# Optimization experiments

Measured on AMD Instinct MI355X. Metric: run time of the kernel, lower is better.

## Reference

```python
import jax, jax.numpy as jnp
import numpy as np

D = 196  # input_size
B = 262144

def _lrelu(x):
    return jax.nn.leaky_relu(x, 0.1)

def setup_inputs() -> dict:
    key = jax.random.key(0)
    ks = jax.random.split(key, 24)
    def w(k, shape):
        fan_in = shape[0]
        return jax.random.uniform(k, shape, jnp.float32, -1.0, 1.0) / np.sqrt(fan_in)
    inp = {}
    inp['x'] = jax.random.normal(ks[0], (B, D), jnp.float32)
    # feature attention: D -> D//2 -> D
    inp['fa_w1'] = w(ks[1], (D, D // 2)); inp['fa_b1'] = jnp.zeros((D // 2,), jnp.float32)
    inp['fa_w2'] = w(ks[2], (D // 2, D)); inp['fa_b2'] = jnp.zeros((D,), jnp.float32)
    # encoder: D -> 96 -> 64 -> 32 -> (8 mean, 8 logvar)
    inp['e_w1'] = w(ks[3], (D, 96)); inp['e_b1'] = jnp.zeros((96,), jnp.float32)
    inp['e_w2'] = w(ks[4], (96, 64)); inp['e_b2'] = jnp.zeros((64,), jnp.float32)
    inp['e_w3'] = w(ks[5], (64, 32)); inp['e_b3'] = jnp.zeros((32,), jnp.float32)
    inp['e_wm'] = w(ks[6], (32, 8)); inp['e_bm'] = jnp.zeros((8,), jnp.float32)
    inp['e_wv'] = w(ks[7], (32, 8)); inp['e_bv'] = jnp.zeros((8,), jnp.float32)
    # decoder: 8 -> 32 -> 64 -> 96 -> D
    inp['d_w1'] = w(ks[8], (8, 32)); inp['d_b1'] = jnp.zeros((32,), jnp.float32)
    inp['d_w2'] = w(ks[9], (32, 64)); inp['d_b2'] = jnp.zeros((64,), jnp.float32)
    inp['d_w3'] = w(ks[10], (64, 96)); inp['d_b3'] = jnp.zeros((96,), jnp.float32)
    inp['d_w4'] = w(ks[11], (96, D)); inp['d_b4'] = jnp.zeros((D,), jnp.float32)
    # layer attention: 3 -> 3 + softmax
    inp['la_w'] = w(ks[12], (3, 3)); inp['la_b'] = jnp.zeros((3,), jnp.float32)
    return inp

def _decoder(z, d_w1, d_b1, d_w2, d_b2, d_w3, d_b3, d_w4, d_b4):
    z = _lrelu(z @ d_w1 + d_b1)
    z = _lrelu(z @ d_w2 + d_b2)
    z = _lrelu(z @ d_w3 + d_b3)
    return jax.nn.sigmoid(z @ d_w4 + d_b4)

def reference(x, fa_w1, fa_b1, fa_w2, fa_b2,
              e_w1, e_b1, e_w2, e_b2, e_w3, e_b3, e_wm, e_bm, e_wv, e_bv,
              d_w1, d_b1, d_w2, d_b2, d_w3, d_b3, d_w4, d_b4,
              la_w, la_b):
    # feature attention
    a = jax.nn.sigmoid(jnp.tanh(x @ fa_w1 + fa_b1) @ fa_w2 + fa_b2)
    attn_weights = a / (jnp.mean(a, axis=1, keepdims=True) + 1e-8)
    x_attn = x * attn_weights
    # encoder
    h1 = _lrelu(x_attn @ e_w1 + e_b1)   # [B,96]
    h2 = _lrelu(h1 @ e_w2 + e_b2)       # [B,64]
    h3 = _lrelu(h2 @ e_w3 + e_b3)       # [B,32]
    mean = h3 @ e_wm + e_bm             # [B,8]
    log_var = h3 @ e_wv + e_bv          # [B,8]
    std = jnp.exp(0.5 * log_var)
    # reparameterize (fresh eps per call, matching torch.randn_like per call)
    ek = jax.random.split(jax.random.key(42), 4)
    z = mean + jax.random.normal(ek[0], mean.shape, mean.dtype) * std
    recon = _decoder(z, d_w1, d_b1, d_w2, d_b2, d_w3, d_b3, d_w4, d_b4)
    # per-layer losses: decoder re-invoked with fresh reparam each time
    layer_losses = []
    for i, h in enumerate((h1, h2, h3)):
        zi = mean + jax.random.normal(ek[i + 1], mean.shape, mean.dtype) * std
        lr = _decoder(zi, d_w1, d_b1, d_w2, d_b2, d_w3, d_b3, d_w4, d_b4)
        layer_losses.append(jnp.mean((h - lr[:, :h.shape[1]]) ** 2, axis=1))
    layer_losses = jnp.stack(layer_losses, axis=1)  # [B,3]
    layer_attn = jax.nn.softmax(layer_losses @ la_w + la_b, axis=-1)
    weighted_layer_loss = jnp.mean(jnp.sum(layer_losses * layer_attn, axis=1))
    return (recon, mean, log_var, attn_weights, weighted_layer_loss)
```

## Files before the change

kernel.cpp:

```cpp
#include <hip/hip_runtime.h>
#include <cstdint>
#include <cstddef>


typedef short short8 __attribute__((ext_vector_type(8)));
typedef float f32x4  __attribute__((ext_vector_type(4)));
typedef float f32x16 __attribute__((ext_vector_type(16)));
typedef unsigned short u16x4 __attribute__((ext_vector_type(4)));
typedef uint32_t u32x2 __attribute__((ext_vector_type(2)));

static constexpr size_t OFF_RECON = 0;
static constexpr size_t OFF_MEAN  = (size_t)262144 * 196;
static constexpr size_t OFF_LOGV  = OFF_MEAN + (size_t)262144 * 8;
static constexpr size_t OFF_ATTN  = OFF_LOGV + (size_t)262144 * 8;
static constexpr size_t OFF_LOSS  = OFF_ATTN + (size_t)262144 * 196;

static constexpr int WS_FA1 = 0;
static constexpr int WS_FA2 = 26624;
static constexpr int WS_E1  = 51712;
static constexpr int WS_E2  = 71680;
static constexpr int WS_E3  = 78848;
static constexpr int WS_EMV = 81408;
static constexpr int WS_D1  = 82944;
static constexpr int WS_D2  = 83456;
static constexpr int WS_D3  = 86528;
static constexpr int WS_D4  = 94208;
static constexpr int WS_TOT = 119296;

static constexpr int XA0 = 0;
static constexpr int T0  = 6656;
static constexpr int TA0 = 10240;
static constexpr int Zo  = 0;
static constexpr int D1o = 2048;
static constexpr int D2o = 5120;
static constexpr int D3o = 10240;
static constexpr int H1o = 17408;
static constexpr int H2o = 20992;
static constexpr int H3o = 23552;
static constexpr int SU_TOT = 25088;

static constexpr int SF_MEAN = 0;
static constexpr int SF_STD  = 256;
static constexpr int SF_ATT  = 512;
static constexpr int SF_LL   = 544;
static constexpr int SF_TOT  = 640;

static constexpr unsigned short BF_ONE = 0x3F80;

struct Params {
  const float* x;
  const float* fa_w1; const float* fa_b1; const float* fa_w2; const float* fa_b2;
  const float* e_w1;  const float* e_b1;  const float* e_w2;  const float* e_b2;
  const float* e_w3;  const float* e_b3;  const float* e_wm;  const float* e_bm;
  const float* e_wv;  const float* e_bv;
  const float* d_w1;  const float* d_b1;  const float* d_w2;  const float* d_b2;
  const float* d_w3;  const float* d_b3;  const float* d_w4;  const float* d_b4;
  const float* la_w;  const float* la_b;
  float* out;
  uint32_t key[8];
};

__host__ __device__ inline void tf2x32(uint32_t k0, uint32_t k1, uint32_t x0, uint32_t x1,
                                       uint32_t& o0, uint32_t& o1)
{
  uint32_t kx = k0 ^ k1 ^ 0x1BD11BDAu;
  uint32_t a = x0 + k0, b = x1 + k1;
#define TF_R(r) { a += b; b = (b << (r)) | (b >> (32 - (r))); b ^= a; }
  TF_R(13) TF_R(15) TF_R(26) TF_R(6)
  a += k1; b += kx + 1u;
  TF_R(17) TF_R(29) TF_R(16) TF_R(24)
  a += kx; b += k0 + 2u;
  TF_R(13) TF_R(15) TF_R(26) TF_R(6)
  a += k0; b += k1 + 3u;
  TF_R(17) TF_R(29) TF_R(16) TF_R(24)
  a += k1; b += kx + 4u;
  TF_R(13) TF_R(15) TF_R(26) TF_R(6)
  a += kx; b += k0 + 5u;
#undef TF_R
  o0 = a; o1 = b;
}

__device__ __forceinline__ float jax_normal(uint32_t k0, uint32_t k1, uint32_t idx)
{
  uint32_t o0, o1;
  tf2x32(k0, k1, 0u, idx, o0, o1);
  uint32_t bits = o0 ^ o1;
  float f = __uint_as_float((bits >> 9) | 0x3f800000u) - 1.0f;
  const float lo = -0.99999994f;
  float u = fmaf(f, 2.0f, lo);
  u = fmaxf(u, lo);
  float w = -log1pf(-u * u);
  float p;
  if (w < 5.0f) {
    w -= 2.5f;
    p = 2.81022636e-08f;
    p = fmaf(p, w, 3.43273939e-07f);
    p = fmaf(p, w, -3.5233877e-06f);
    p = fmaf(p, w, -4.39150654e-06f);
    p = fmaf(p, w, 0.00021858087f);
    p = fmaf(p, w, -0.00125372503f);
    p = fmaf(p, w, -0.00417768164f);
    p = fmaf(p, w, 0.246640727f);
    p = fmaf(p, w, 1.50140941f);
  } else {
    w = sqrtf(w) - 3.0f;
    p = -0.000200214257f;
    p = fmaf(p, w, 0.000100950558f);
    p = fmaf(p, w, 0.00134934322f);
    p = fmaf(p, w, -0.00367342844f);
    p = fmaf(p, w, 0.00573950773f);
    p = fmaf(p, w, -0.0076224613f);
    p = fmaf(p, w, 0.00943887047f);
    p = fmaf(p, w, 1.00167406f);
    p = fmaf(p, w, 2.83297682f);
  }
  return 1.41421356237f * (p * u);
}

__host__ __device__ __forceinline__ unsigned short f2b(float f) {
  uint32_t u = __float_as_uint(f);
  uint32_t r = u + 0x7fffu + ((u >> 16) & 1u);
  return (unsigned short)(r >> 16);
}
__device__ __forceinline__ float b2f(unsigned short hh) {
  return __uint_as_float(((uint32_t)hh) << 16);
}
__device__ __forceinline__ uint32_t cvt_pk(float lo, float hi) {
  uint32_t r;
  asm("v_cvt_pk_bf16_f32 %0, %1, %2" : "=v"(r) : "v"(lo), "v"(hi));
  return r;
}
__device__ __forceinline__ float rcpf(float x) { return __builtin_amdgcn_rcpf(x); }
__device__ __forceinline__ float sigm(float x) { return rcpf(1.0f + __expf(-x)); }
__device__ __forceinline__ float tanh_fast(float x) {
  float xc = fminf(fmaxf(x, -8.0f), 8.0f);
  float t = __expf(2.0f * xc);
  return (t - 1.0f) * rcpf(t + 1.0f);
}

__global__ void pack_w(Params p, unsigned short* ws)
{
  int e = blockIdx.x * 256 + threadIdx.x;
  if (e >= WS_TOT) return;
  int base, KS, K, N, special = 0;
  const float* src = nullptr; const float* bias = nullptr;
  if (e < WS_FA2)      { base = WS_FA1; KS = 13; K = 196; N = 98;  src = p.fa_w1; bias = p.fa_b1; }
  else if (e < WS_E1)  { base = WS_FA2; KS = 7;  K = 98;  N = 196; src = p.fa_w2; bias = p.fa_b2; }
  else if (e < WS_E2)  { base = WS_E1;  KS = 13; K = 196; N = 96;  src = p.e_w1;  bias = p.e_b1; }
  else if (e < WS_E3)  { base = WS_E2;  KS = 7;  K = 96;  N = 64;  src = p.e_w2;  bias = p.e_b2; }
  else if (e < WS_EMV) { base = WS_E3;  KS = 5;  K = 64;  N = 32;  src = p.e_w3;  bias = p.e_b3; }
  else if (e < WS_D1)  { base = WS_EMV; KS = 3;  K = 32;  N = 16;  special = 1; }
  else if (e < WS_D2)  { base = WS_D1;  KS = 1;  K = 8;   N = 32;  src = p.d_w1;  bias = p.d_b1; }
  else if (e < WS_D3)  { base = WS_D2;  KS = 3;  K = 32;  N = 64;  src = p.d_w2;  bias = p.d_b2; }
  else if (e < WS_D4)  { base = WS_D3;  KS = 5;  K = 64;  N = 96;  src = p.d_w3;  bias = p.d_b3; }
  else                 { base = WS_D4;  KS = 7;  K = 96;  N = 196; src = p.d_w4;  bias = p.d_b4; }
  int local = e - base;
  int j = local & 7, lane = (local >> 3) & 63, t = local >> 9;
  int ksi = t % KS, ft = t / KS;
  int k = ksi * 16 + ((lane >> 5) << 3) + j;
  int n = ft * 32 + (lane & 31);
  float v = 0.f;
  if (n < N) {
    if (k < K)       v = special ? ((n < 8) ? p.e_wm[k * 8 + n] : p.e_wv[k * 8 + (n - 8)])
                                 : src[k * N + n];
    else if (k == K) v = special ? ((n < 8) ? p.e_bm[n] : p.e_bv[n - 8]) : bias[n];
  }
  ws[e] = f2b(v);
}

template<int KS>
__device__ __forceinline__ f32x16 tile32(const unsigned short* A, int sA,
                                         const unsigned short* W, int ft, int lane)
{
  f32x16 acc = {};
  const unsigned short* ar = A + (lane & 31) * sA + ((lane >> 5) << 3);
  const unsigned short* wp = W + (size_t)(ft * KS * 64 + lane) * 8;
#pragma unroll
  for (int ks = 0; ks < KS; ++ks) {
    short8 bv  = *(const short8*)(ar + ks * 16);
    short8 wv8 = *(const short8*)(wp + ks * 512);
    acc = __builtin_amdgcn_mfma_f32_32x32x16_bf16(wv8, bv, acc, 0, 0, 0);
  }
  return acc;
}

template<int KS, int MT, int NFT>
__device__ __forceinline__ void layer32(unsigned short* sUb, int aOff, int sA,
                                        int dOff, int sD,
                                        const unsigned short* W, int lane, int wv)
{
  const int m = lane & 31, h = lane >> 5;
  for (int t = wv; t < MT * NFT; t += 4) {
    int mt = (MT == 1) ? 0 : (t & (MT - 1));
    int ft = (MT == 1) ? t : (t >> (MT == 2 ? 1 : 0));
    f32x16 acc = tile32<KS>(sUb + aOff + mt * 32 * sA, sA, W, ft, lane);
    int rr = mt * 32 + m;
#pragma unroll
    for (int g = 0; g < 4; ++g) {
      float v0 = fmaxf(acc[4*g+0], 0.1f * acc[4*g+0]);
      float v1 = fmaxf(acc[4*g+1], 0.1f * acc[4*g+1]);
      float v2 = fmaxf(acc[4*g+2], 0.1f * acc[4*g+2]);
      float v3 = fmaxf(acc[4*g+3], 0.1f * acc[4*g+3]);
      u32x2 pk = { cvt_pk(v0, v1), cvt_pk(v2, v3) };
      *(u32x2*)&sUb[dOff + rr * sD + ft * 32 + 8 * g + 4 * h] = pk;
    }
  }
}

__launch_bounds__(256, 3)
__global__ void vae_fused(Params p, const unsigned short* ws)
{
  __shared__ unsigned short sU[SU_TOT];
  __shared__ float sF[SF_TOT];
  unsigned short* sUb = sU;

  const int tid = threadIdx.x;
  const int lane = tid & 63;
  const int wv = tid >> 6;
  const int m = lane & 31;
  const int h = lane >> 5;
  const int rb0 = blockIdx.x * 32;

  if (tid < 128) sF[SF_ATT + tid] = 0.f;
  for (int idx = tid; idx < 1568; idx += 256) {
    int row = idx / 49, q = idx - row * 49;
    f32x4 xv = *(const f32x4*)(p.x + (size_t)(rb0 + row) * 196 + 4 * q);
    u32x2 pk = { cvt_pk(xv[0], xv[1]), cvt_pk(xv[2], xv[3]) };
    *(u32x2*)&sUb[XA0 + row * 208 + 4 * q] = pk;
  }
  if (tid < 32) {
    unsigned short* r = sUb + XA0 + tid * 208;
    r[196] = BF_ONE; r[197] = 0; r[198] = 0; r[199] = 0;
    u16x4 z4 = {0, 0, 0, 0};
    *(u16x4*)&r[200] = z4; *(u16x4*)&r[204] = z4;
  }
  __syncthreads();

  {
    int ft = wv;
    f32x16 acc = tile32<13>(sUb + XA0, 208, ws + WS_FA1, ft, lane);
    if (ft < 3) {
#pragma unroll
      for (int g = 0; g < 4; ++g) {
        float v0 = tanh_fast(acc[4*g+0]), v1 = tanh_fast(acc[4*g+1]);
        float v2 = tanh_fast(acc[4*g+2]), v3 = tanh_fast(acc[4*g+3]);
        u32x2 pk = { cvt_pk(v0, v1), cvt_pk(v2, v3) };
        *(u32x2*)&sUb[T0 + m * 112 + ft * 32 + 8 * g + 4 * h] = pk;
      }
    } else if (h == 0) {
      *(uint32_t*)&sUb[T0 + m * 112 + 96] = cvt_pk(tanh_fast(acc[0]), tanh_fast(acc[1]));
    }
    if (tid < 32) {
      unsigned short* r = sUb + T0 + tid * 112;
      r[98] = BF_ONE; r[99] = 0;
      u16x4 z4 = {0, 0, 0, 0};
      *(u16x4*)&r[100] = z4; *(u16x4*)&r[104] = z4; *(u16x4*)&r[108] = z4;
    }
  }
  __syncthreads();

  for (int ft = wv; ft < 7; ft += 4) {
    f32x16 acc = tile32<7>(sUb + T0, 112, ws + WS_FA2, ft, lane);
    float s = 0.f;
#pragma unroll
    for (int g = 0; g < 4; ++g) {
      int fb = ft * 32 + 8 * g + 4 * h;
      if (fb <= 192) {
        float a0 = sigm(acc[4*g+0]), a1 = sigm(acc[4*g+1]);
        float a2 = sigm(acc[4*g+2]), a3 = sigm(acc[4*g+3]);
        s += a0 + a1 + a2 + a3;
        u32x2 pk = { cvt_pk(a0, a1), cvt_pk(a2, a3) };
        *(u32x2*)&sUb[TA0 + m * 200 + fb] = pk;
      }
    }
    s += __shfl_xor(s, 32, 64);
    if (lane < 32) atomicAdd(&sF[SF_ATT + m], s);
  }
  __syncthreads();

  for (int idx = tid; idx < 1568; idx += 256) {
    int row = idx / 49, q = idx - row * 49;
    float inv = rcpf(sF[SF_ATT + row] * (1.0f / 196.0f) + 1e-8f);
    u16x4 ah = *(const u16x4*)&sUb[TA0 + row * 200 + 4 * q];
    u16x4 xh = *(const u16x4*)&sUb[XA0 + row * 208 + 4 * q];
    f32x4 aw;
    float xo[4];
#pragma unroll
    for (int i = 0; i < 4; ++i) {
      aw[i] = b2f(ah[i]) * inv;
      xo[i] = b2f(xh[i]) * aw[i];
    }
    __builtin_nontemporal_store(aw, (f32x4*)(p.out + OFF_ATTN + (size_t)(rb0 + row) * 196 + 4 * q));
    u32x2 pk = { cvt_pk(xo[0], xo[1]), cvt_pk(xo[2], xo[3]) };
    *(u32x2*)&sUb[XA0 + row * 208 + 4 * q] = pk;
  }
  __syncthreads();

  layer32<13, 1, 3>(sUb, XA0, 208, H1o, 112, ws + WS_E1, lane, wv);
  if (tid < 32) {
    unsigned short* r = sUb + H1o + tid * 112;
    r[96] = BF_ONE; r[97] = 0; r[98] = 0; r[99] = 0;
    u16x4 z4 = {0, 0, 0, 0};
    *(u16x4*)&r[100] = z4; *(u16x4*)&r[104] = z4; *(u16x4*)&r[108] = z4;
  }
  __syncthreads();
  layer32<7, 1, 2>(sUb, H1o, 112, H2o, 80, ws + WS_E2, lane, wv);
  if (tid < 32) {
    unsigned short* r = sUb + H2o + tid * 80;
    r[64] = BF_ONE; r[65] = 0; r[66] = 0; r[67] = 0;
    u16x4 z4 = {0, 0, 0, 0};
    *(u16x4*)&r[68] = z4; *(u16x4*)&r[72] = z4; *(u16x4*)&r[76] = z4;
  }
  __syncthreads();
  layer32<5, 1, 1>(sUb, H2o, 80, H3o, 48, ws + WS_E3, lane, wv);
  if (tid < 32) {
    unsigned short* r = sUb + H3o + tid * 48;
    r[32] = BF_ONE; r[33] = 0; r[34] = 0; r[35] = 0;
    u16x4 z4 = {0, 0, 0, 0};
    *(u16x4*)&r[36] = z4; *(u16x4*)&r[40] = z4; *(u16x4*)&r[44] = z4;
  }
  __syncthreads();

  if (wv == 0) {
    f32x16 acc = tile32<3>(sUb + H3o, 48, ws + WS_EMV, 0, lane);
    f32x4 mv, lv;
#pragma unroll
    for (int e = 0; e < 4; ++e) { mv[e] = acc[e]; lv[e] = acc[4 + e]; }
#pragma unroll
    for (int e = 0; e < 4; ++e) {
      sF[SF_MEAN + m * 8 + 4 * h + e] = mv[e];
      sF[SF_STD  + m * 8 + 4 * h + e] = __expf(0.5f * lv[e]);
    }
    __builtin_nontemporal_store(mv, (f32x4*)(p.out + OFF_MEAN + (size_t)(rb0 + m) * 8 + 4 * h));
    __builtin_nontemporal_store(lv, (f32x4*)(p.out + OFF_LOGV + (size_t)(rb0 + m) * 8 + 4 * h));
  }
  __syncthreads();

  {
    int r = tid >> 1, half = tid & 1;
    int draw = r >> 5, row = r & 31;
    float z[4];
#pragma unroll
    for (int e = 0; e < 4; ++e) {
      int jj = 4 * half + e;
      float eps = jax_normal(p.key[2 * draw], p.key[2 * draw + 1],
                             (uint32_t)(rb0 + row) * 8u + (uint32_t)jj);
      z[e] = fmaf(eps, sF[SF_STD + row * 8 + jj], sF[SF_MEAN + row * 8 + jj]);
    }
    u32x2 pk = { cvt_pk(z[0], z[1]), cvt_pk(z[2], z[3]) };
    *(u32x2*)&sUb[Zo + r * 16 + 4 * half] = pk;
    if (tid < 128) {
      u16x4 one4 = {BF_ONE, 0, 0, 0}, z4 = {0, 0, 0, 0};
      *(u16x4*)&sUb[Zo + tid * 16 + 8]  = one4;
      *(u16x4*)&sUb[Zo + tid * 16 + 12] = z4;
    }
  }
  __syncthreads();

#pragma unroll
  for (int pass = 0; pass < 2; ++pass) {
    const int zr = pass * 64;
    layer32<1, 2, 1>(sUb, Zo + zr * 16, 16, D1o, 48, ws + WS_D1, lane, wv);
    if (pass == 0 && tid < 64) {
      unsigned short* r = sUb + D1o + tid * 48;
      r[32] = BF_ONE; r[33] = 0; r[34] = 0; r[35] = 0;
      u16x4 z4 = {0, 0, 0, 0};
      *(u16x4*)&r[36] = z4; *(u16x4*)&r[40] = z4; *(u16x4*)&r[44] = z4;
    }
    __syncthreads();
    layer32<3, 2, 2>(sUb, D1o, 48, D2o, 80, ws + WS_D2, lane, wv);
    if (pass == 0 && tid < 64) {
      unsigned short* r = sUb + D2o + tid * 80;
      r[64] = BF_ONE; r[65] = 0; r[66] = 0; r[67] = 0;
      u16x4 z4 = {0, 0, 0, 0};
      *(u16x4*)&r[68] = z4; *(u16x4*)&r[72] = z4; *(u16x4*)&r[76] = z4;
    }
    __syncthreads();
    layer32<5, 2, 3>(sUb, D2o, 80, D3o, 112, ws + WS_D3, lane, wv);
    if (pass == 0 && tid < 64) {
      unsigned short* r = sUb + D3o + tid * 112;
      r[96] = BF_ONE; r[97] = 0; r[98] = 0; r[99] = 0;
      u16x4 z4 = {0, 0, 0, 0};
      *(u16x4*)&r[100] = z4; *(u16x4*)&r[104] = z4; *(u16x4*)&r[108] = z4;
    }
    __syncthreads();

    auto d4_loss = [&](int dp, int ft, int hOff, int sH, float invD, int li) {
      f32x16 acc = tile32<7>(sUb + D3o + dp * 32 * 112, 112, ws + WS_D4, ft, lane);
      float s = 0.f;
#pragma unroll
      for (int g = 0; g < 4; ++g) {
        int fb = ft * 32 + 8 * g + 4 * h;
        u16x4 hh = *(const u16x4*)&sUb[hOff + m * sH + fb];
#pragma unroll
        for (int e = 0; e < 4; ++e) {
          float lr = sigm(acc[4 * g + e]);
          float d = b2f(hh[e]) - lr;
          s = fmaf(d, d, s);
        }
      }
      s += __shfl_xor(s, 32, 64);
      if (lane < 32) atomicAdd(&sF[SF_LL + li * 32 + m], s * invD);
    };

    if (pass == 0) {
      for (int t = wv; t < 10; t += 4) {
        if (t < 7) {
          f32x16 acc = tile32<7>(sUb + D3o, 112, ws + WS_D4, t, lane);
#pragma unroll
          for (int g = 0; g < 4; ++g) {
            int fb = t * 32 + 8 * g + 4 * h;
            if (fb <= 192) {
              f32x4 v;
#pragma unroll
              for (int e = 0; e < 4; ++e) v[e] = sigm(acc[4 * g + e]);
              __builtin_nontemporal_store(v,
                  (f32x4*)(p.out + OFF_RECON + (size_t)(rb0 + m) * 196 + fb));
            }
          }
        } else {
          d4_loss(1, t - 7, H1o, 112, 1.0f / 96.0f, 0);
        }
      }
    } else {
      for (int t = wv; t < 3; t += 4) {
        if (t < 2) d4_loss(0, t, H2o, 80, 1.0f / 64.0f, 1);
        else       d4_loss(1, 0, H3o, 48, 1.0f / 32.0f, 2);
      }
    }
    __syncthreads();
  }

  if (tid < 32) {
    int r = tid;
    float l0 = sF[SF_LL + r], l1 = sF[SF_LL + 32 + r], l2 = sF[SF_LL + 64 + r];
    float lg[3];
#pragma unroll
    for (int i = 0; i < 3; ++i)
      lg[i] = p.la_b[i] + l0 * p.la_w[0 * 3 + i] + l1 * p.la_w[1 * 3 + i] + l2 * p.la_w[2 * 3 + i];
    float mx = fmaxf(lg[0], fmaxf(lg[1], lg[2]));
    float e0 = __expf(lg[0] - mx), e1 = __expf(lg[1] - mx), e2 = __expf(lg[2] - mx);
    float inv = rcpf(e0 + e1 + e2);
    float wll = (l0 * e0 + l1 * e1 + l2 * e2) * inv;
#pragma unroll
    for (int mm = 1; mm <= 16; mm <<= 1) wll += __shfl_xor(wll, mm, 64);
    if (tid == 0) atomicAdd(p.out + OFF_LOSS, wll * (1.0f / 262144.0f));
  }
}

extern "C" void kernel_launch(void* const* d_in, const int* in_sizes, int n_in,
                              void* d_out, int out_size, void* d_ws, size_t ws_size,
                              hipStream_t stream)
{
  (void)in_sizes; (void)n_in; (void)ws_size; (void)out_size;
  Params p;
  p.x     = (const float*)d_in[0];
  p.fa_w1 = (const float*)d_in[1];  p.fa_b1 = (const float*)d_in[2];
  p.fa_w2 = (const float*)d_in[3];  p.fa_b2 = (const float*)d_in[4];
  p.e_w1  = (const float*)d_in[5];  p.e_b1  = (const float*)d_in[6];
  p.e_w2  = (const float*)d_in[7];  p.e_b2  = (const float*)d_in[8];
  p.e_w3  = (const float*)d_in[9];  p.e_b3  = (const float*)d_in[10];
  p.e_wm  = (const float*)d_in[11]; p.e_bm  = (const float*)d_in[12];
  p.e_wv  = (const float*)d_in[13]; p.e_bv  = (const float*)d_in[14];
  p.d_w1  = (const float*)d_in[15]; p.d_b1  = (const float*)d_in[16];
  p.d_w2  = (const float*)d_in[17]; p.d_b2  = (const float*)d_in[18];
  p.d_w3  = (const float*)d_in[19]; p.d_b3  = (const float*)d_in[20];
  p.d_w4  = (const float*)d_in[21]; p.d_b4  = (const float*)d_in[22];
  p.la_w  = (const float*)d_in[23]; p.la_b  = (const float*)d_in[24];
  p.out   = (float*)d_out;

  for (uint32_t j = 0; j < 4; ++j) {
    uint32_t o0, o1;
    tf2x32(0u, 42u, 0u, j, o0, o1);
    p.key[2 * j] = o0; p.key[2 * j + 1] = o1;
  }

  hipMemsetAsync((char*)d_out + OFF_LOSS * sizeof(float), 0, sizeof(float), stream);

  unsigned short* ws = (unsigned short*)d_ws;
  pack_w<<<(WS_TOT + 255) / 256, 256, 0, stream>>>(p, ws);
  vae_fused<<<262144 / 32, 256, 0, stream>>>(p, ws);
}
```

Baseline: 352.1 us.

## Shrink LDS footprint, pipeline decoder draws one at a time, raise occupancy

Reorganizes shared memory by aliasing encoder and decoder buffers and processing the four decoder draws one 32-row tile at a time instead of two 64-row passes. This cuts LDS use so the launch bound can rise from 3 to 4 blocks per CU. The next draw's first decoder layer is overlapped with the current draw's output layer, and eps generation is hoisted ahead of a barrier. Long-K MFMA chains now alternate between two accumulators to break the dependency. In exchange there are more barriers per block and a risk of register pressure or spills under the tighter bound.

New measurement: 355.3 us. About the same (+0.9%).

```diff
diff --git a/kernel.cpp b/kernel.cpp
--- a/kernel.cpp
+++ b/kernel.cpp
@@ -28,22 +28,18 @@
 static constexpr int WS_TOT = 119296;
 
 static constexpr int XA0 = 0;
-static constexpr int T0  = 6656;
-static constexpr int TA0 = 10240;
-static constexpr int Zo  = 0;
-static constexpr int D1o = 2048;
-static constexpr int D2o = 5120;
-static constexpr int D3o = 10240;
-static constexpr int H1o = 17408;
-static constexpr int H2o = 20992;
-static constexpr int H3o = 23552;
-static constexpr int SU_TOT = 25088;
-
-static constexpr int SF_MEAN = 0;
-static constexpr int SF_STD  = 256;
-static constexpr int SF_ATT  = 512;
-static constexpr int SF_LL   = 544;
-static constexpr int SF_TOT  = 640;
+static constexpr int T0  = 6912;
+static constexpr int TA0 = 10752;
+static constexpr int H1o = 6912;
+static constexpr int H2o = 10752;
+static constexpr int H3o = 13568;
+static constexpr int D1o = 15360;
+static constexpr int D2o = 3840;
+static constexpr int D3o = 0;
+static constexpr int Zo  = 17152;
+static constexpr int SU_TOT = 19200;
+static constexpr int SF_MEAN = 0, SF_STD = 256, SF_ATT = 512, SF_LL = 544;
+static constexpr int SF_TOT = 640;
 
 static constexpr unsigned short BF_ONE = 0x3F80;
 
@@ -172,47 +168,45 @@
 __device__ __forceinline__ f32x16 tile32(const unsigned short* A, int sA,
                                          const unsigned short* W, int ft, int lane)
 {
-  f32x16 acc = {};
+  f32x16 a0 = {}, a1 = {};
   const unsigned short* ar = A + (lane & 31) * sA + ((lane >> 5) << 3);
   const unsigned short* wp = W + (size_t)(ft * KS * 64 + lane) * 8;
 #pragma unroll
   for (int ks = 0; ks < KS; ++ks) {
     short8 bv  = *(const short8*)(ar + ks * 16);
     short8 wv8 = *(const short8*)(wp + ks * 512);
-    acc = __builtin_amdgcn_mfma_f32_32x32x16_bf16(wv8, bv, acc, 0, 0, 0);
-  }
-  return acc;
-}
-
-template<int KS, int MT, int NFT>
-__device__ __forceinline__ void layer32(unsigned short* sUb, int aOff, int sA,
-                                        int dOff, int sD,
-                                        const unsigned short* W, int lane, int wv)
+    if (KS >= 7 && (ks & 1)) a1 = __builtin_amdgcn_mfma_f32_32x32x16_bf16(wv8, bv, a1, 0, 0, 0);
+    else                     a0 = __builtin_amdgcn_mfma_f32_32x32x16_bf16(wv8, bv, a0, 0, 0, 0);
+  }
+  if (KS >= 7) a0 += a1;
+  return a0;
+}
+
+template<int KS, int NFT, int SA, int SD>
+__device__ __forceinline__ void layer_lrelu(unsigned short* sU, int aOff, int dOff,
+                                            const unsigned short* W, int lane, int wv)
 {
   const int m = lane & 31, h = lane >> 5;
-  for (int t = wv; t < MT * NFT; t += 4) {
-    int mt = (MT == 1) ? 0 : (t & (MT - 1));
-    int ft = (MT == 1) ? t : (t >> (MT == 2 ? 1 : 0));
-    f32x16 acc = tile32<KS>(sUb + aOff + mt * 32 * sA, sA, W, ft, lane);
-    int rr = mt * 32 + m;
-#pragma unroll
-    for (int g = 0; g < 4; ++g) {
-      float v0 = fmaxf(acc[4*g+0], 0.1f * acc[4*g+0]);
-      float v1 = fmaxf(acc[4*g+1], 0.1f * acc[4*g+1]);
-      float v2 = fmaxf(acc[4*g+2], 0.1f * acc[4*g+2]);
-      float v3 = fmaxf(acc[4*g+3], 0.1f * acc[4*g+3]);
+  for (int t = wv; t < NFT; t += 4) {
+    f32x16 acc = tile32<KS>(sU + aOff, SA, W, t, lane);
+#pragma unroll
+    for (int g = 0; g < 4; ++g) {
+      int fb = t * 32 + 8 * g + 4 * h;
+      float v0 = fmaxf(acc[4*g+0], 0.1f*acc[4*g+0]);
+      float v1 = fmaxf(acc[4*g+1], 0.1f*acc[4*g+1]);
+      float v2 = fmaxf(acc[4*g+2], 0.1f*acc[4*g+2]);
+      float v3 = fmaxf(acc[4*g+3], 0.1f*acc[4*g+3]);
       u32x2 pk = { cvt_pk(v0, v1), cvt_pk(v2, v3) };
-      *(u32x2*)&sUb[dOff + rr * sD + ft * 32 + 8 * g + 4 * h] = pk;
-    }
-  }
-}
-
-__launch_bounds__(256, 3)
+      *(u32x2*)&sU[dOff + m * SD + fb] = pk;
+    }
+  }
+}
+
+__launch_bounds__(256, 4)
 __global__ void vae_fused(Params p, const unsigned short* ws)
 {
   __shared__ unsigned short sU[SU_TOT];
   __shared__ float sF[SF_TOT];
-  unsigned short* sUb = sU;
 
   const int tid = threadIdx.x;
   const int lane = tid & 63;
@@ -221,56 +215,57 @@
   const int h = lane >> 5;
   const int rb0 = blockIdx.x * 32;
 
+  const u16x4 one4 = {BF_ONE, 0, 0, 0};
+  const u16x4 zr4  = {0, 0, 0, 0};
+
   if (tid < 128) sF[SF_ATT + tid] = 0.f;
   for (int idx = tid; idx < 1568; idx += 256) {
     int row = idx / 49, q = idx - row * 49;
     f32x4 xv = *(const f32x4*)(p.x + (size_t)(rb0 + row) * 196 + 4 * q);
     u32x2 pk = { cvt_pk(xv[0], xv[1]), cvt_pk(xv[2], xv[3]) };
-    *(u32x2*)&sUb[XA0 + row * 208 + 4 * q] = pk;
-  }
-  if (tid < 32) {
-    unsigned short* r = sUb + XA0 + tid * 208;
-    r[196] = BF_ONE; r[197] = 0; r[198] = 0; r[199] = 0;
-    u16x4 z4 = {0, 0, 0, 0};
-    *(u16x4*)&r[200] = z4; *(u16x4*)&r[204] = z4;
+    *(u32x2*)&sU[XA0 + row * 216 + 4 * q] = pk;
+  }
+  if (tid < 32) {
+    unsigned short* r = sU + XA0 + tid * 216;
+    *(u16x4*)&r[196] = one4; *(u16x4*)&r[200] = zr4; *(u16x4*)&r[204] = zr4;
+  }
+  if (tid < 128) {
+    unsigned short* r = sU + Zo + tid * 16;
+    *(u16x4*)&r[8] = one4; *(u16x4*)&r[12] = zr4;
   }
   __syncthreads();
 
   {
-    int ft = wv;
-    f32x16 acc = tile32<13>(sUb + XA0, 208, ws + WS_FA1, ft, lane);
-    if (ft < 3) {
-#pragma unroll
-      for (int g = 0; g < 4; ++g) {
-        float v0 = tanh_fast(acc[4*g+0]), v1 = tanh_fast(acc[4*g+1]);
-        float v2 = tanh_fast(acc[4*g+2]), v3 = tanh_fast(acc[4*g+3]);
+    int t = wv;
+    f32x16 acc = tile32<13>(sU + XA0, 216, ws + WS_FA1, t, lane);
+#pragma unroll
+    for (int g = 0; g < 4; ++g) {
+      int fb = t * 32 + 8 * g + 4 * h;
+      if (fb + 4 <= 120) {
+        float v0 = tanh_fast(acc[4*g+0]);
+        float v1 = tanh_fast(acc[4*g+1]);
+        float v2 = tanh_fast(acc[4*g+2]);
+        float v3 = tanh_fast(acc[4*g+3]);
+        if (fb == 96) v2 = 1.0f;
         u32x2 pk = { cvt_pk(v0, v1), cvt_pk(v2, v3) };
-        *(u32x2*)&sUb[T0 + m * 112 + ft * 32 + 8 * g + 4 * h] = pk;
+        *(u32x2*)&sU[T0 + m * 120 + fb] = pk;
       }
-    } else if (h == 0) {
-      *(uint32_t*)&sUb[T0 + m * 112 + 96] = cvt_pk(tanh_fast(acc[0]), tanh_fast(acc[1]));
-    }
-    if (tid < 32) {
-      unsigned short* r = sUb + T0 + tid * 112;
-      r[98] = BF_ONE; r[99] = 0;
-      u16x4 z4 = {0, 0, 0, 0};
-      *(u16x4*)&r[100] = z4; *(u16x4*)&r[104] = z4; *(u16x4*)&r[108] = z4;
-    }
-  }
-  __syncthreads();
-
-  for (int ft = wv; ft < 7; ft += 4) {
-    f32x16 acc = tile32<7>(sUb + T0, 112, ws + WS_FA2, ft, lane);
+    }
+  }
+  __syncthreads();
+
+  for (int t = wv; t < 7; t += 4) {
+    f32x16 acc = tile32<7>(sU + T0, 120, ws + WS_FA2, t, lane);
     float s = 0.f;
 #pragma unroll
     for (int g = 0; g < 4; ++g) {
-      int fb = ft * 32 + 8 * g + 4 * h;
-      if (fb <= 192) {
+      int fb = t * 32 + 8 * g + 4 * h;
+      if (fb + 4 <= 200) {
         float a0 = sigm(acc[4*g+0]), a1 = sigm(acc[4*g+1]);
         float a2 = sigm(acc[4*g+2]), a3 = sigm(acc[4*g+3]);
-        s += a0 + a1 + a2 + a3;
+        if (fb < 196) s += a0 + a1 + a2 + a3;
         u32x2 pk = { cvt_pk(a0, a1), cvt_pk(a2, a3) };
-        *(u32x2*)&sUb[TA0 + m * 200 + fb] = pk;
+        *(u32x2*)&sU[TA0 + m * 200 + fb] = pk;
       }
     }
     s += __shfl_xor(s, 32, 64);
@@ -281,8 +276,8 @@
   for (int idx = tid; idx < 1568; idx += 256) {
     int row = idx / 49, q = idx - row * 49;
     float inv = rcpf(sF[SF_ATT + row] * (1.0f / 196.0f) + 1e-8f);
-    u16x4 ah = *(const u16x4*)&sUb[TA0 + row * 200 + 4 * q];
-    u16x4 xh = *(const u16x4*)&sUb[XA0 + row * 208 + 4 * q];
+    u16x4 ah = *(const u16x4*)&sU[TA0 + row * 200 + 4 * q];
+    u16x4 xh = *(const u16x4*)&sU[XA0 + row * 216 + 4 * q];
     f32x4 aw;
     float xo[4];
 #pragma unroll
@@ -292,37 +287,34 @@
     }
     __builtin_nontemporal_store(aw, (f32x4*)(p.out + OFF_ATTN + (size_t)(rb0 + row) * 196 + 4 * q));
     u32x2 pk = { cvt_pk(xo[0], xo[1]), cvt_pk(xo[2], xo[3]) };
-    *(u32x2*)&sUb[XA0 + row * 208 + 4 * q] = pk;
-  }
-  __syncthreads();
-
-  layer32<13, 1, 3>(sUb, XA0, 208, H1o, 112, ws + WS_E1, lane, wv);
-  if (tid < 32) {
-    unsigned short* r = sUb + H1o + tid * 112;
-    r[96] = BF_ONE; r[97] = 0; r[98] = 0; r[99] = 0;
-    u16x4 z4 = {0, 0, 0, 0};
-    *(u16x4*)&r[100] = z4; *(u16x4*)&r[104] = z4; *(u16x4*)&r[108] = z4;
-  }
-  __syncthreads();
-  layer32<7, 1, 2>(sUb, H1o, 112, H2o, 80, ws + WS_E2, lane, wv);
-  if (tid < 32) {
-    unsigned short* r = sUb + H2o + tid * 80;
-    r[64] = BF_ONE; r[65] = 0; r[66] = 0; r[67] = 0;
-    u16x4 z4 = {0, 0, 0, 0};
-    *(u16x4*)&r[68] = z4; *(u16x4*)&r[72] = z4; *(u16x4*)&r[76] = z4;
-  }
-  __syncthreads();
-  layer32<5, 1, 1>(sUb, H2o, 80, H3o, 48, ws + WS_E3, lane, wv);
-  if (tid < 32) {
-    unsigned short* r = sUb + H3o + tid * 48;
-    r[32] = BF_ONE; r[33] = 0; r[34] = 0; r[35] = 0;
-    u16x4 z4 = {0, 0, 0, 0};
-    *(u16x4*)&r[36] = z4; *(u16x4*)&r[40] = z4; *(u16x4*)&r[44] = z4;
+    *(u32x2*)&sU[XA0 + row * 216 + 4 * q] = pk;
+  }
+  __syncthreads();
+
+  layer_lrelu<13, 3, 216, 120>(sU, XA0, H1o, ws + WS_E1, lane, wv);
+  if (tid < 32) {
+    unsigned short* r = sU + H1o + tid * 120;
+    *(u16x4*)&r[96] = one4; *(u16x4*)&r[100] = zr4;
+    *(u16x4*)&r[104] = zr4; *(u16x4*)&r[108] = zr4;
+  }
+  __syncthreads();
+  layer_lrelu<7, 2, 120, 88>(sU, H1o, H2o, ws + WS_E2, lane, wv);
+  if (tid < 32) {
+    unsigned short* r = sU + H2o + tid * 88;
+    *(u16x4*)&r[64] = one4; *(u16x4*)&r[68] = zr4;
+    *(u16x4*)&r[72] = zr4;  *(u16x4*)&r[76] = zr4;
+  }
+  __syncthreads();
+  layer_lrelu<5, 1, 88, 56>(sU, H2o, H3o, ws + WS_E3, lane, wv);
+  if (tid < 32) {
+    unsigned short* r = sU + H3o + tid * 56;
+    *(u16x4*)&r[32] = one4; *(u16x4*)&r[36] = zr4;
+    *(u16x4*)&r[40] = zr4;  *(u16x4*)&r[44] = zr4;
   }
   __syncthreads();
 
   if (wv == 0) {
-    f32x16 acc = tile32<3>(sUb + H3o, 48, ws + WS_EMV, 0, lane);
+    f32x16 acc = tile32<3>(sU + H3o, 56, ws + WS_EMV, 0, lane);
     f32x4 mv, lv;
 #pragma unroll
     for (int e = 0; e < 4; ++e) { mv[e] = acc[e]; lv[e] = acc[4 + e]; }
@@ -334,99 +326,104 @@
     __builtin_nontemporal_store(mv, (f32x4*)(p.out + OFF_MEAN + (size_t)(rb0 + m) * 8 + 4 * h));
     __builtin_nontemporal_store(lv, (f32x4*)(p.out + OFF_LOGV + (size_t)(rb0 + m) * 8 + 4 * h));
   }
-  __syncthreads();
-
+  if (tid < 32) {
+    unsigned short* r1 = sU + D1o + tid * 56;
+    *(u16x4*)&r1[32] = one4; *(u16x4*)&r1[36] = zr4;
+    *(u16x4*)&r1[40] = zr4;  *(u16x4*)&r1[44] = zr4;
+    unsigned short* r2 = sU + D2o + tid * 88;
+    *(u16x4*)&r2[64] = one4; *(u16x4*)&r2[68] = zr4;
+    *(u16x4*)&r2[72] = zr4;  *(u16x4*)&r2[76] = zr4;
+    unsigned short* r3 = sU + D3o + tid * 120;
+    *(u16x4*)&r3[96] = one4; *(u16x4*)&r3[100] = zr4;
+    *(u16x4*)&r3[104] = zr4; *(u16x4*)&r3[108] = zr4;
+  }
+  float eps4[4];
   {
-    int r = tid >> 1, half = tid & 1;
-    int draw = r >> 5, row = r & 31;
-    float z[4];
+    const int row = (tid >> 1) & 31;
+    const uint32_t k0 = p.key[2 * wv], k1 = p.key[2 * wv + 1];
+#pragma unroll
+    for (int e = 0; e < 4; ++e)
+      eps4[e] = jax_normal(k0, k1, (uint32_t)(rb0 + row) * 8u + 4 * (tid & 1) + e);
+  }
+  __syncthreads();
+
+  auto dec_d1 = [&](int dr) {
+    f32x16 acc = tile32<1>(sU + Zo + dr * 32 * 16, 16, ws + WS_D1, 0, lane);
+#pragma unroll
+    for (int g = 0; g < 4; ++g) {
+      int fb = 8 * g + 4 * h;
+      float v0 = fmaxf(acc[4*g+0], 0.1f*acc[4*g+0]);
+      float v1 = fmaxf(acc[4*g+1], 0.1f*acc[4*g+1]);
+      float v2 = fmaxf(acc[4*g+2], 0.1f*acc[4*g+2]);
+      float v3 = fmaxf(acc[4*g+3], 0.1f*acc[4*g+3]);
+      u32x2 pk = { cvt_pk(v0, v1), cvt_pk(v2, v3) };
+      *(u32x2*)&sU[D1o + m * 56 + fb] = pk;
+    }
+  };
+  auto d4_recon = [&](int t) {
+    f32x16 acc = tile32<7>(sU + D3o, 120, ws + WS_D4, t, lane);
+#pragma unroll
+    for (int g = 0; g < 4; ++g) {
+      int fb = t * 32 + 8 * g + 4 * h;
+      if (fb <= 192) {
+        f32x4 v;
+#pragma unroll
+        for (int e = 0; e < 4; ++e) v[e] = sigm(acc[4 * g + e]);
+        __builtin_nontemporal_store(v, (f32x4*)(p.out + OFF_RECON + (size_t)(rb0 + m) * 196 + fb));
+      }
+    }
+  };
+  auto d4_loss = [&](int t, int hOff, int sH, float invD, int li) {
+    f32x16 acc = tile32<7>(sU + D3o, 120, ws + WS_D4, t, lane);
+    float s = 0.f;
+#pragma unroll
+    for (int g = 0; g < 4; ++g) {
+      int fb = t * 32 + 8 * g + 4 * h;
+      u16x4 hh = *(const u16x4*)&sU[hOff + m * sH + fb];
+#pragma unroll
+      for (int e = 0; e < 4; ++e) {
+        float lr = sigm(acc[4 * g + e]);
+        float dd = b2f(hh[e]) - lr;
+        s = fmaf(dd, dd, s);
+      }
+    }
+    s += __shfl_xor(s, 32, 64);
+    if (lane < 32) atomicAdd(&sF[SF_LL + li * 32 + m], s * invD);
+  };
+
+  {
+    const int r = tid >> 1, half = tid & 1, row = r & 31;
+    f32x4 zv;
 #pragma unroll
     for (int e = 0; e < 4; ++e) {
       int jj = 4 * half + e;
-      float eps = jax_normal(p.key[2 * draw], p.key[2 * draw + 1],
-                             (uint32_t)(rb0 + row) * 8u + (uint32_t)jj);
-      z[e] = fmaf(eps, sF[SF_STD + row * 8 + jj], sF[SF_MEAN + row * 8 + jj]);
-    }
-    u32x2 pk = { cvt_pk(z[0], z[1]), cvt_pk(z[2], z[3]) };
-    *(u32x2*)&sUb[Zo + r * 16 + 4 * half] = pk;
-    if (tid < 128) {
-      u16x4 one4 = {BF_ONE, 0, 0, 0}, z4 = {0, 0, 0, 0};
-      *(u16x4*)&sUb[Zo + tid * 16 + 8]  = one4;
-      *(u16x4*)&sUb[Zo + tid * 16 + 12] = z4;
-    }
-  }
-  __syncthreads();
-
-#pragma unroll
-  for (int pass = 0; pass < 2; ++pass) {
-    const int zr = pass * 64;
-    layer32<1, 2, 1>(sUb, Zo + zr * 16, 16, D1o, 48, ws + WS_D1, lane, wv);
-    if (pass == 0 && tid < 64) {
-      unsigned short* r = sUb + D1o + tid * 48;
-      r[32] = BF_ONE; r[33] = 0; r[34] = 0; r[35] = 0;
-      u16x4 z4 = {0, 0, 0, 0};
-      *(u16x4*)&r[36] = z4; *(u16x4*)&r[40] = z4; *(u16x4*)&r[44] = z4;
-    }
+      zv[e] = fmaf(eps4[e], sF[SF_STD + row * 8 + jj], sF[SF_MEAN + row * 8 + jj]);
+    }
+    u32x2 pk = { cvt_pk(zv[0], zv[1]), cvt_pk(zv[2], zv[3]) };
+    *(u32x2*)&sU[Zo + r * 16 + 4 * half] = pk;
+  }
+  if (wv == 0) dec_d1(0);
+  __syncthreads();
+
+#pragma unroll
+  for (int d = 0; d < 4; ++d) {
+    layer_lrelu<3, 2, 56, 88>(sU, D1o, D2o, ws + WS_D2, lane, wv);
     __syncthreads();
-    layer32<3, 2, 2>(sUb, D1o, 48, D2o, 80, ws + WS_D2, lane, wv);
-    if (pass == 0 && tid < 64) {
-      unsigned short* r = sUb + D2o + tid * 80;
-      r[64] = BF_ONE; r[65] = 0; r[66] = 0; r[67] = 0;
-      u16x4 z4 = {0, 0, 0, 0};
-      *(u16x4*)&r[68] = z4; *(u16x4*)&r[72] = z4; *(u16x4*)&r[76] = z4;
-    }
+    layer_lrelu<5, 3, 88, 120>(sU, D2o, D3o, ws + WS_D3, lane, wv);
     __syncthreads();
-    layer32<5, 2, 3>(sUb, D2o, 80, D3o, 112, ws + WS_D3, lane, wv);
-    if (pass == 0 && tid < 64) {
-      unsigned short* r = sUb + D3o + tid * 112;
-      r[96] = BF_ONE; r[97] = 0; r[98] = 0; r[99] = 0;
-      u16x4 z4 = {0, 0, 0, 0};
-      *(u16x4*)&r[100] = z4; *(u16x4*)&r[104] = z4; *(u16x4*)&r[108] = z4;
-    }
-    __syncthreads();
-
-    auto d4_loss = [&](int dp, int ft, int hOff, int sH, float invD, int li) {
-      f32x16 acc = tile32<7>(sUb + D3o + dp * 32 * 112, 112, ws + WS_D4, ft, lane);
-      float s = 0.f;
-#pragma unroll
-      for (int g = 0; g < 4; ++g) {
-        int fb = ft * 32 + 8 * g + 4 * h;
-        u16x4 hh = *(const u16x4*)&sUb[hOff + m * sH + fb];
-#pragma unroll
-        for (int e = 0; e < 4; ++e) {
-          float lr = sigm(acc[4 * g + e]);
-          float d = b2f(hh[e]) - lr;
-          s = fmaf(d, d, s);
-        }
+    if (d == 0) {
+      for (int t = wv; t < 8; t += 4) {
+        if (t < 7) d4_recon(t);
+        else       dec_d1(1);
       }
-      s += __shfl_xor(s, 32, 64);
-      if (lane < 32) atomicAdd(&sF[SF_LL + li * 32 + m], s * invD);
-    };
-
-    if (pass == 0) {
-      for (int t = wv; t < 10; t += 4) {
-        if (t < 7) {
-          f32x16 acc = tile32<7>(sUb + D3o, 112, ws + WS_D4, t, lane);
-#pragma unroll
-          for (int g = 0; g < 4; ++g) {
-            int fb = t * 32 + 8 * g + 4 * h;
-            if (fb <= 192) {
-              f32x4 v;
-#pragma unroll
-              for (int e = 0; e < 4; ++e) v[e] = sigm(acc[4 * g + e]);
-              __builtin_nontemporal_store(v,
-                  (f32x4*)(p.out + OFF_RECON + (size_t)(rb0 + m) * 196 + fb));
-            }
-          }
-        } else {
-          d4_loss(1, t - 7, H1o, 112, 1.0f / 96.0f, 0);
-        }
-      }
+    } else if (d == 1) {
+      if (wv < 3) d4_loss(wv, H1o, 120, 1.0f / 96.0f, 0);
+      else        dec_d1(2);
+    } else if (d == 2) {
+      if (wv < 2)       d4_loss(wv, H2o, 88, 1.0f / 64.0f, 1);
+      else if (wv == 2) dec_d1(3);
     } else {
-      for (int t = wv; t < 3; t += 4) {
-        if (t < 2) d4_loss(0, t, H2o, 80, 1.0f / 64.0f, 1);
-        else       d4_loss(1, 0, H3o, 48, 1.0f / 32.0f, 2);
-      }
+      if (wv == 0) d4_loss(0, H3o, 56, 1.0f / 32.0f, 2);
     }
     __syncthreads();
   }
```
